# Optimization experiments

Measured on AMD Instinct MI355X. Metric: run time of the kernel, lower is better.

Reference implementation:

```python
import jax, jax.numpy as jnp
import numpy as np

N = 200000      # active voxels
G = 256         # dense grid extent per axis
C = 64          # inc = cs[0] at cr=1.0
S = 8           # aux pooling scale -> 32^3 aux cells
GS = G // S
NSEG = GS * GS * GS
EPS = 1e-6


def layernorm(x, w, b):
    m = jnp.mean(x, axis=-1, keepdims=True)
    v = jnp.mean((x - m) ** 2, axis=-1, keepdims=True)
    return (x - m) / jnp.sqrt(v + EPS) * w + b


def setup_inputs() -> dict:
    key = jax.random.key(0)
    ks = jax.random.split(key, 8)
    # unique voxel coordinates in a 256^3 grid (batch idx last, = 0)
    rng = np.random.default_rng(0)
    lin = rng.choice(G ** 3, size=N, replace=False).astype(np.int64)
    x = (lin // (G * G)).astype(np.int32)
    y = ((lin // G) % G).astype(np.int32)
    z = (lin % G).astype(np.int32)
    coords = jnp.asarray(np.stack([x, y, z, np.zeros(N, np.int32)], axis=1))
    feats = jax.random.normal(ks[0], (N, C), dtype=jnp.float32)
    return {
        "feats": feats,
        "W_pre": jax.random.normal(ks[1], (C, C), dtype=jnp.float32) * 0.05,
        "ln_pre_w": jnp.ones((C,), jnp.float32),
        "ln_pre_b": jnp.zeros((C,), jnp.float32),
        "W_pos": jax.random.normal(ks[2], (C, 3), dtype=jnp.float32) * 0.05,
        "alpha": jnp.ones((1, C), jnp.float32),
        "conv_w": jax.random.normal(ks[3], (27, C, C), dtype=jnp.float32) * 0.02,
        "ln_w": jnp.ones((C,), jnp.float32),
        "ln_b": jnp.zeros((C,), jnp.float32),
        "lnl_w": jnp.ones((C,), jnp.float32),
        "lnl_b": jnp.zeros((C,), jnp.float32),
        "coords": coords,
    }


def _elk_forward(feats, W_pre, ln_pre_w, ln_pre_b, W_pos, alpha, conv_w,
                 ln_w, ln_b, lnl_w, lnl_b, coords):
    xyz = coords[:, :3]
    # pre_mix: Linear(no bias) + LayerNorm
    F_input = layernorm(feats @ W_pre.T, ln_pre_w, ln_pre_b)
    # pos_weight = Linear(3->C, no bias)(xyz) * alpha (baseop='cos_x', groups=1)
    pos = (xyz.astype(jnp.float32) @ W_pos.T) * alpha          # [N, C]
    p_sin = jnp.sin(pos)
    p_cos = jnp.cos(pos)
    Fw_lin = F_input * pos
    # local_mix: 3x3x3 sparse conv on original feats via hash-grid gather
    gx, gy, gz = xyz[:, 0], xyz[:, 1], xyz[:, 2]
    grid = jnp.full((G, G, G), -1, jnp.int32).at[gx, gy, gz].set(
        jnp.arange(N, dtype=jnp.int32))
    local = jnp.zeros((N, C), jnp.float32)
    k = 0
    for dx in (-1, 0, 1):
        for dy in (-1, 0, 1):
            for dz in (-1, 0, 1):
                nc = xyz + jnp.array([dx, dy, dz], jnp.int32)
                inb = jnp.all((nc >= 0) & (nc < G), axis=1)
                ncc = jnp.clip(nc, 0, G - 1)
                nidx = grid[ncc[:, 0], ncc[:, 1], ncc[:, 2]]
                valid = inb & (nidx >= 0)
                g = jnp.where(valid[:, None],
                              feats[jnp.maximum(nidx, 0)], 0.0)
                local = local + g @ conv_w[k]
                k += 1
    # voxel_to_aux: scatter-pool the concat [cos*F, sin*F, pos*F] to aux cells
    stF = jnp.concatenate([F_input * p_cos, F_input * p_sin, Fw_lin], axis=1)
    cell = xyz // S
    seg = (cell[:, 0] * GS + cell[:, 1]) * GS + cell[:, 2]    # [N]
    sums = jax.ops.segment_sum(stF, seg, num_segments=NSEG)   # [NSEG, 3C]
    counts = jax.ops.segment_sum(jnp.ones((N,), jnp.float32), seg,
                                 num_segments=NSEG)
    # aux_to_voxel: broadcast aux mean back to each voxel
    vox = sums[seg] / jnp.maximum(counts[seg], 1.0)[:, None]  # [N, 3C]
    new_F = (vox[:, :C] * p_cos + vox[:, C:2 * C] * p_sin
             + (vox[:, 2 * C:] - Fw_lin))
    out = jax.nn.relu(layernorm(new_F, ln_w, ln_b)
                      + layernorm(local, lnl_w, lnl_b))
    return out


def reference(feats, W_pre, ln_pre_w, ln_pre_b, W_pos, alpha, conv_w,
              ln_w, ln_b, lnl_w, lnl_b, coords):
    return _elk_forward(feats, W_pre, ln_pre_w, ln_pre_b, W_pos, alpha,
                        conv_w, ln_w, ln_b, lnl_w, lnl_b, coords)
```

## Files before the change

### kernel.cpp

```cpp
#include <hip/hip_runtime.h>


typedef unsigned int u32;
typedef unsigned long long u64;

#define EPSV 1e-6f
#define HBITS 19
#define HSIZE (1u << HBITS)
#define HMASK (HSIZE - 1u)
#define CAP 32
#define PAD 65

template<int C,int R> __device__ __forceinline__ float dpp_add(float x){
    int y = __builtin_amdgcn_update_dpp(0, __float_as_int(x), C, R, 0xf, true);
    return x + __int_as_float(y);
}
__device__ __forceinline__ float wave_sum(float x){
    x = dpp_add<0xB1,0xF>(x);
    x = dpp_add<0x4E,0xF>(x);
    x = dpp_add<0x141,0xF>(x);
    x = dpp_add<0x140,0xF>(x);
    x = dpp_add<0x142,0xA>(x);
    x = dpp_add<0x143,0xC>(x);
    return __int_as_float(__builtin_amdgcn_readlane(__float_as_int(x), 63));
}
__device__ __forceinline__ void wave_sum2(float& x, float& y){
    x = dpp_add<0xB1,0xF>(x);   y = dpp_add<0xB1,0xF>(y);
    x = dpp_add<0x4E,0xF>(x);   y = dpp_add<0x4E,0xF>(y);
    x = dpp_add<0x141,0xF>(x);  y = dpp_add<0x141,0xF>(y);
    x = dpp_add<0x140,0xF>(x);  y = dpp_add<0x140,0xF>(y);
    x = dpp_add<0x142,0xA>(x);  y = dpp_add<0x142,0xA>(y);
    x = dpp_add<0x143,0xC>(x);  y = dpp_add<0x143,0xC>(y);
    x = __int_as_float(__builtin_amdgcn_readlane(__float_as_int(x), 63));
    y = __int_as_float(__builtin_amdgcn_readlane(__float_as_int(y), 63));
}

__device__ __forceinline__ u32 hslot(u32 b){ return (b * 0x9E3779B1u) >> (32 - HBITS); }

__global__ void k_scatter(const int* __restrict__ coords, u64* __restrict__ hash,
                          u32* __restrict__ bm, int n){
    int i = blockIdx.x * blockDim.x + threadIdx.x;
    if(i < n){
        int4 c = ((const int4*)coords)[i];
        u32 b = ((u32)c.x << 16) | ((u32)c.y << 8) | (u32)c.z;
        atomicOr(&bm[b >> 5], 1u << (b & 31));
        u64 entry = ((u64)b << 32) | (u32)i;
        u32 s = hslot(b);
        while(atomicCAS(&hash[s], ~0ull, entry) != ~0ull) s = (s + 1) & HMASK;
    }
}

__global__ void k_wtr(const float* __restrict__ W_pre, float* __restrict__ WT){
    for(int idx = threadIdx.x; idx < 4096; idx += 256){
        int j = idx >> 6, c = idx & 63;
        WT[j*64 + c] = W_pre[c*64 + j];
    }
}

__launch_bounds__(256, 2)
__global__ void k_preT(const float* __restrict__ feats, const float* __restrict__ WT,
                       const float* __restrict__ conv_w,
                       const float* __restrict__ lnw, const float* __restrict__ lnb,
                       float* __restrict__ F_input, float* __restrict__ selfconv, int n){
    __shared__ float T[64 * PAD];
    __shared__ float redm[4][64];
    __shared__ float redv[4][64];

    const int tid  = threadIdx.x;
    const int lane = tid & 63;
    const int wid  = tid >> 6;
    const int tbase = blockIdx.x << 6;

#pragma unroll
    for(int r = 0; r < 4; ++r){
        int idx = (r << 8) + tid;
        int pt = idx >> 4, j4 = idx & 15;
        float4 v = make_float4(0.f,0.f,0.f,0.f);
        if(tbase + pt < n) v = ((const float4*)feats)[(size_t)(tbase + pt) * 16 + j4];
        T[(4*j4 + 0)*PAD + pt] = v.x;
        T[(4*j4 + 1)*PAD + pt] = v.y;
        T[(4*j4 + 2)*PAD + pt] = v.z;
        T[(4*j4 + 3)*PAD + pt] = v.w;
    }
    __syncthreads();

    const int c0 = __builtin_amdgcn_readfirstlane(wid) << 4;
    const float* wa = WT + c0;
    const float* wb = conv_w + 13*4096 + c0;

    float accA[16], accB[16];
#pragma unroll
    for(int cc = 0; cc < 16; ++cc){ accA[cc] = 0.f; accB[cc] = 0.f; }

#pragma unroll 4
    for(int j = 0; j < 64; ++j){
        float v = T[j*PAD + lane];
        const float* waj = wa + j*64;
        const float* wbj = wb + j*64;
#pragma unroll
        for(int cc = 0; cc < 16; ++cc){
            accA[cc] = fmaf(v, waj[cc], accA[cc]);
            accB[cc] = fmaf(v, wbj[cc], accB[cc]);
        }
    }

    float s = 0.f;
#pragma unroll
    for(int cc = 0; cc < 16; ++cc) s += accA[cc];
    redm[wid][lane] = s;
    __syncthreads();
    const float mean = (redm[0][lane] + redm[1][lane] + redm[2][lane] + redm[3][lane]) * (1.f/64.f);
    float vs = 0.f;
#pragma unroll
    for(int cc = 0; cc < 16; ++cc){ float d = accA[cc] - mean; vs = fmaf(d, d, vs); }
    redv[wid][lane] = vs;
    __syncthreads();
    const float var = (redv[0][lane] + redv[1][lane] + redv[2][lane] + redv[3][lane]) * (1.f/64.f);
    const float rs = rsqrtf(var + EPSV);

#pragma unroll
    for(int cc = 0; cc < 16; ++cc)
        T[(c0 + cc)*PAD + lane] = (accA[cc] - mean) * rs * lnw[c0 + cc] + lnb[c0 + cc];
    __syncthreads();
#pragma unroll
    for(int r = 0; r < 4; ++r){
        int idx = (r << 8) + tid;
        int pt = idx >> 4, g = idx & 15;
        if(tbase + pt < n){
            float4 v = make_float4(T[(4*g+0)*PAD + pt], T[(4*g+1)*PAD + pt],
                                   T[(4*g+2)*PAD + pt], T[(4*g+3)*PAD + pt]);
            ((float4*)F_input)[(size_t)(tbase + pt) * 16 + g] = v;
        }
    }
    __syncthreads();

#pragma unroll
    for(int cc = 0; cc < 16; ++cc)
        T[(c0 + cc)*PAD + lane] = accB[cc];
    __syncthreads();
#pragma unroll
    for(int r = 0; r < 4; ++r){
        int idx = (r << 8) + tid;
        int pt = idx >> 4, g = idx & 15;
        if(tbase + pt < n){
            float4 v = make_float4(T[(4*g+0)*PAD + pt], T[(4*g+1)*PAD + pt],
                                   T[(4*g+2)*PAD + pt], T[(4*g+3)*PAD + pt]);
            ((float4*)selfconv)[(size_t)(tbase + pt) * 16 + g] = v;
        }
    }
}

__launch_bounds__(256)
__global__ void k_segfinal(const float* __restrict__ F_input,
                           const float* __restrict__ selfconv,
                           const float* __restrict__ feats,
                           const float* __restrict__ W_pos, const float* __restrict__ alpha,
                           const float* __restrict__ conv_w,
                           const float* __restrict__ ln_w, const float* __restrict__ ln_b,
                           const float* __restrict__ lnl_w, const float* __restrict__ lnl_b,
                           const u64* __restrict__ hash, const u32* __restrict__ bm,
                           float* __restrict__ out){
    __shared__ u32   s_pid[4][CAP];
    __shared__ u32   s_cell[4][CAP];
    __shared__ float s_v[4][3][64];
    __shared__ int   s_np[4];

    const u64* bm64 = (const u64*)bm;
    const int lane = threadIdx.x & 63;
    const int wid  = threadIdx.x >> 6;
    const int seg  = (blockIdx.x << 2) + wid;
    const int cx = seg >> 10, cy = (seg >> 5) & 31, cz = seg & 31;

    const int px = (cx << 3) + (lane >> 3), py = (cy << 3) + (lane & 7);
    u64 w = bm64[((size_t)px << 10) | ((u32)py << 2) | (u32)(cz >> 3)];
    u32 o8 = (u32)(w >> ((cz & 7) * 8)) & 0xffu;

    const float wx = W_pos[lane*3+0], wy = W_pos[lane*3+1], wz = W_pos[lane*3+2];
    const float al = alpha[lane];

    float aC = 0.f, aS = 0.f, aL = 0.f;
    int np = 0;
    float cnt = wave_sum((float)__popc(o8));
    u32 t8 = o8;
    while(__ballot(t8 != 0u)){
        int myz = 0, pid = -1;
        if(t8){
            int dz = __ffs(t8) - 1; t8 &= t8 - 1;
            myz = (cz << 3) + dz;
            u32 b = ((u32)px << 16) | ((u32)py << 8) | (u32)myz;
            u32 s = hslot(b); u64 e;
            while((u32)((e = hash[s]) >> 32) != b) s = (s + 1) & HMASK;
            pid = (int)(u32)e;
        }
        u64 mm = __ballot(pid >= 0);
        while(mm){
            int l = __ffsll(mm) - 1; mm &= mm - 1;
            int p  = __builtin_amdgcn_readlane(pid, l);
            int pz = __builtin_amdgcn_readlane(myz, l);
            int qx = (cx << 3) + (l >> 3), qy = (cy << 3) + (l & 7);
            if(np < CAP && lane == 0){
                s_pid[wid][np]  = (u32)p;
                s_cell[wid][np] = ((u32)qx << 16) | ((u32)qy << 8) | (u32)pz;
            }
            ++np;
            float F = F_input[(size_t)p * 64 + lane];
            float pos = ((float)qx*wx + (float)qy*wy + (float)pz*wz) * al;
            aC = fmaf(F, __cosf(pos), aC);
            aS = fmaf(F, __sinf(pos), aS);
            aL = fmaf(F, pos, aL);
        }
    }
    const float inv = 1.f / fmaxf(cnt, 1.f);
    s_v[wid][0][lane] = aC * inv;
    s_v[wid][1][lane] = aS * inv;
    s_v[wid][2][lane] = aL * inv;
    if(lane == 0) s_np[wid] = np < CAP ? np : CAP;
    __syncthreads();

    const float lnwv = ln_w[lane], lnbv = ln_b[lane];
    const float llwv = lnl_w[lane], llbv = lnl_b[lane];

    const int np0 = s_np[0], np1 = s_np[1], np2 = s_np[2], np3 = s_np[3];
    const int c01 = np0 + np1, c012 = c01 + np2;
    const int tot = c012 + np3;

    for(int idx = wid; idx < tot; idx += 4){
        int s, p;
        if(idx < np0){ s = 0; p = idx; }
        else if(idx < c01){ s = 1; p = idx - np0; }
        else if(idx < c012){ s = 2; p = idx - c01; }
        else { s = 3; p = idx - c012; }
        const u32 pid  = s_pid[s][p];
        const u32 cell = s_cell[s][p];
        const int qx = (int)(cell >> 16), qy = (int)((cell >> 8) & 255u), pz = (int)(cell & 255u);
        const float vCv = s_v[s][0][lane], vSv = s_v[s][1][lane], vLv = s_v[s][2][lane];

        float F  = F_input[(size_t)pid * 64 + lane];
        float Sc = selfconv[(size_t)pid * 64 + lane];

        u32 m3 = 0;
        if(lane < 9){
            int nx = qx + lane/3 - 1, ny = qy + lane%3 - 1;
            if(((u32)nx < 256u) && ((u32)ny < 256u)){
                const u64* wp = bm64 + (((size_t)nx << 10) | ((u32)ny << 2));
                int zb = pz & 63;
                if(zb >= 1 && zb <= 62){
                    u64 ww = wp[pz >> 6];
                    m3 = (u32)((ww >> (zb - 1)) & 7ull);
                } else {
#pragma unroll
                    for(int t = 0; t < 3; ++t){
                        int zz = pz + t - 1;
                        if((u32)zz < 256u){
                            u64 ww = wp[zz >> 6];
                            m3 |= (u32)((ww >> (zz & 63)) & 1ull) << t;
                        }
                    }
                }
            }
        }
        u64 b0m = __ballot(m3 & 1u);
        u64 b1m = __ballot(m3 & 2u) & ~(1ull << 4);
        u64 b2m = __ballot(m3 & 4u);

        float pos = ((float)qx*wx + (float)qy*wy + (float)pz*wz) * al;
        float sn = __sinf(pos), cs = __cosf(pos);
        float newF = fmaf(vCv, cs, fmaf(vSv, sn, vLv - F*pos));
        float local = Sc;

#pragma unroll
        for(int t = 0; t < 3; ++t){
            u64 mm2 = (t == 0) ? b0m : ((t == 1) ? b1m : b2m);
            while(mm2){
                int l2 = __ffsll(mm2) - 1; mm2 &= mm2 - 1;
                int nx = qx + l2/3 - 1, ny = qy + l2%3 - 1, nz = pz + t - 1;
                int k = 3*l2 + t;
                u32 nb = ((u32)nx << 16) | ((u32)ny << 8) | (u32)nz;
                u32 s2 = hslot(nb); u64 e;
                while((u32)((e = hash[s2]) >> 32) != nb) s2 = (s2 + 1) & HMASK;
                const int pin = (int)(u32)e;
                const float4* gv = (const float4*)(feats + (size_t)pin * 64);
                const float* cwp = conv_w + (size_t)k * 4096;
#pragma unroll 4
                for(int q = 0; q < 16; ++q){
                    float4 g = gv[q];
                    local = fmaf(g.x, cwp[(4*q    )*64 + lane], local);
                    local = fmaf(g.y, cwp[(4*q + 1)*64 + lane], local);
                    local = fmaf(g.z, cwp[(4*q + 2)*64 + lane], local);
                    local = fmaf(g.w, cwp[(4*q + 3)*64 + lane], local);
                }
            }
        }

        float m1 = newF, m2 = local;
        wave_sum2(m1, m2); m1 *= (1.f/64.f); m2 *= (1.f/64.f);
        float t1 = newF - m1, t2 = local - m2;
        float v1 = t1*t1, v2 = t2*t2;
        wave_sum2(v1, v2); v1 *= (1.f/64.f); v2 *= (1.f/64.f);
        float a1 = t1 * rsqrtf(v1 + EPSV) * lnwv + lnbv;
        float a2 = t2 * rsqrtf(v2 + EPSV) * llwv + llbv;

        out[(size_t)pid*64 + lane] = fmaxf(a1 + a2, 0.f);
    }
}

extern "C" void kernel_launch(void* const* d_in, const int* in_sizes, int n_in,
                              void* d_out, int out_size, void* d_ws, size_t ws_size,
                              hipStream_t stream) {
    (void)n_in; (void)out_size; (void)ws_size;
    const float* feats    = (const float*)d_in[0];
    const float* W_pre    = (const float*)d_in[1];
    const float* ln_pre_w = (const float*)d_in[2];
    const float* ln_pre_b = (const float*)d_in[3];
    const float* W_pos    = (const float*)d_in[4];
    const float* alpha    = (const float*)d_in[5];
    const float* conv_w   = (const float*)d_in[6];
    const float* ln_w     = (const float*)d_in[7];
    const float* ln_b     = (const float*)d_in[8];
    const float* lnl_w    = (const float*)d_in[9];
    const float* lnl_b    = (const float*)d_in[10];
    const int*   coords   = (const int*)d_in[11];

    const int n = in_sizes[0] / 64;

    char* ws = (char*)d_ws;
    size_t o = 0;
    u64*   hash    = (u64*)(ws + o);   o += (size_t)HSIZE * 8;
    u32*   bm      = (u32*)(ws + o);   o += 2097152;
    float* WT      = (float*)(ws + o); o += 16384;
    float* F_input = (float*)(ws + o); o += (size_t)n * 256;
    float* selfconv= (float*)(ws + o); o += (size_t)n * 256;

    hipMemsetAsync(hash, 0xFF, (size_t)HSIZE * 8, stream);
    hipMemsetAsync(bm, 0, 2097152, stream);

    k_wtr<<<1, 256, 0, stream>>>(W_pre, WT);
    k_scatter<<<(n + 255)/256, 256, 0, stream>>>(coords, hash, bm, n);
    k_preT<<<(n + 63)/64, 256, 0, stream>>>(feats, WT, conv_w, ln_pre_w, ln_pre_b,
                                            F_input, selfconv, n);
    k_segfinal<<<8192, 256, 0, stream>>>(F_input, selfconv, feats, W_pos, alpha,
                                         conv_w, ln_w, ln_b, lnl_w, lnl_b,
                                         hash, bm, (float*)d_out);
}
```

Measured before the change: 203.8 us.

## Fuse hash build into pre-mix kernel and cache gathered features in LDS

Result: slower. 221.9 us (+8.9%).

```diff
diff --git a/kernel.cpp b/kernel.cpp
--- a/kernel.cpp
+++ b/kernel.cpp
@@ -14,15 +14,6 @@
 template<int C,int R> __device__ __forceinline__ float dpp_add(float x){
     int y = __builtin_amdgcn_update_dpp(0, __float_as_int(x), C, R, 0xf, true);
     return x + __int_as_float(y);
-}
-__device__ __forceinline__ float wave_sum(float x){
-    x = dpp_add<0xB1,0xF>(x);
-    x = dpp_add<0x4E,0xF>(x);
-    x = dpp_add<0x141,0xF>(x);
-    x = dpp_add<0x140,0xF>(x);
-    x = dpp_add<0x142,0xA>(x);
-    x = dpp_add<0x143,0xC>(x);
-    return __int_as_float(__builtin_amdgcn_readlane(__float_as_int(x), 63));
 }
 __device__ __forceinline__ void wave_sum2(float& x, float& y){
     x = dpp_add<0xB1,0xF>(x);   y = dpp_add<0xB1,0xF>(y);
@@ -37,19 +28,6 @@
 
 __device__ __forceinline__ u32 hslot(u32 b){ return (b * 0x9E3779B1u) >> (32 - HBITS); }
 
-__global__ void k_scatter(const int* __restrict__ coords, u64* __restrict__ hash,
-                          u32* __restrict__ bm, int n){
-    int i = blockIdx.x * blockDim.x + threadIdx.x;
-    if(i < n){
-        int4 c = ((const int4*)coords)[i];
-        u32 b = ((u32)c.x << 16) | ((u32)c.y << 8) | (u32)c.z;
-        atomicOr(&bm[b >> 5], 1u << (b & 31));
-        u64 entry = ((u64)b << 32) | (u32)i;
-        u32 s = hslot(b);
-        while(atomicCAS(&hash[s], ~0ull, entry) != ~0ull) s = (s + 1) & HMASK;
-    }
-}
-
 __global__ void k_wtr(const float* __restrict__ W_pre, float* __restrict__ WT){
     for(int idx = threadIdx.x; idx < 4096; idx += 256){
         int j = idx >> 6, c = idx & 63;
@@ -61,6 +39,8 @@
 __global__ void k_preT(const float* __restrict__ feats, const float* __restrict__ WT,
                        const float* __restrict__ conv_w,
                        const float* __restrict__ lnw, const float* __restrict__ lnb,
+                       const int* __restrict__ coords,
+                       u64* __restrict__ hash, u32* __restrict__ bm,
                        float* __restrict__ F_input, float* __restrict__ selfconv, int n){
     __shared__ float T[64 * PAD];
     __shared__ float redm[4][64];
@@ -81,6 +61,15 @@
         T[(4*j4 + 1)*PAD + pt] = v.y;
         T[(4*j4 + 2)*PAD + pt] = v.z;
         T[(4*j4 + 3)*PAD + pt] = v.w;
+    }
+
+    if(tid < 64 && tbase + tid < n){
+        int4 c = ((const int4*)coords)[tbase + tid];
+        u32 b = ((u32)c.x << 16) | ((u32)c.y << 8) | (u32)c.z;
+        atomicOr(&bm[b >> 5], 1u << (b & 31));
+        u64 entry = ((u64)b << 32) | (u32)(tbase + tid);
+        u32 s = hslot(b);
+        while(atomicCAS(&hash[s], ~0ull, entry) != ~0ull) s = (s + 1) & HMASK;
     }
     __syncthreads();
 
@@ -160,6 +149,7 @@
                            const float* __restrict__ lnl_w, const float* __restrict__ lnl_b,
                            const u64* __restrict__ hash, const u32* __restrict__ bm,
                            float* __restrict__ out){
+    __shared__ float s_F[4][CAP][64];
     __shared__ u32   s_pid[4][CAP];
     __shared__ u32   s_cell[4][CAP];
     __shared__ float s_v[4][3][64];
@@ -178,49 +168,52 @@
     const float wx = W_pos[lane*3+0], wy = W_pos[lane*3+1], wz = W_pos[lane*3+2];
     const float al = alpha[lane];
 
+    if(lane == 0) s_np[wid] = 0;
+    __syncthreads();
+
+    u32 t8 = o8;
+    while(t8){
+        int dz = __ffs(t8) - 1; t8 &= t8 - 1;
+        int pz = (cz << 3) + dz;
+        u32 b = ((u32)px << 16) | ((u32)py << 8) | (u32)pz;
+        u32 s = hslot(b); u64 e;
+        while((u32)((e = hash[s]) >> 32) != b) s = (s + 1) & HMASK;
+        int slot = atomicAdd(&s_np[wid], 1);
+        if(slot < CAP){
+            s_pid[wid][slot]  = (u32)e;
+            s_cell[wid][slot] = b;
+        }
+    }
+    __syncthreads();
+
+    const int npAll = s_np[wid];
+    const int np = npAll < CAP ? npAll : CAP;
     float aC = 0.f, aS = 0.f, aL = 0.f;
-    int np = 0;
-    float cnt = wave_sum((float)__popc(o8));
-    u32 t8 = o8;
-    while(__ballot(t8 != 0u)){
-        int myz = 0, pid = -1;
-        if(t8){
-            int dz = __ffs(t8) - 1; t8 &= t8 - 1;
-            myz = (cz << 3) + dz;
-            u32 b = ((u32)px << 16) | ((u32)py << 8) | (u32)myz;
-            u32 s = hslot(b); u64 e;
-            while((u32)((e = hash[s]) >> 32) != b) s = (s + 1) & HMASK;
-            pid = (int)(u32)e;
-        }
-        u64 mm = __ballot(pid >= 0);
-        while(mm){
-            int l = __ffsll(mm) - 1; mm &= mm - 1;
-            int p  = __builtin_amdgcn_readlane(pid, l);
-            int pz = __builtin_amdgcn_readlane(myz, l);
-            int qx = (cx << 3) + (l >> 3), qy = (cy << 3) + (l & 7);
-            if(np < CAP && lane == 0){
-                s_pid[wid][np]  = (u32)p;
-                s_cell[wid][np] = ((u32)qx << 16) | ((u32)qy << 8) | (u32)pz;
-            }
-            ++np;
-            float F = F_input[(size_t)p * 64 + lane];
-            float pos = ((float)qx*wx + (float)qy*wy + (float)pz*wz) * al;
-            aC = fmaf(F, __cosf(pos), aC);
-            aS = fmaf(F, __sinf(pos), aS);
-            aL = fmaf(F, pos, aL);
-        }
-    }
-    const float inv = 1.f / fmaxf(cnt, 1.f);
+#pragma unroll 2
+    for(int p = 0; p < np; ++p){
+        const u32 pid  = s_pid[wid][p];
+        const u32 cell = s_cell[wid][p];
+        const int qx = (int)(cell >> 16), qy = (int)((cell >> 8) & 255u), pz = (int)(cell & 255u);
+        float F = F_input[(size_t)pid * 64 + lane];
+        s_F[wid][p][lane] = F;
+        float pos = ((float)qx*wx + (float)qy*wy + (float)pz*wz) * al;
+        aC = fmaf(F, __cosf(pos), aC);
+        aS = fmaf(F, __sinf(pos), aS);
+        aL = fmaf(F, pos, aL);
+    }
+    const float inv = 1.f / fmaxf((float)npAll, 1.f);
     s_v[wid][0][lane] = aC * inv;
     s_v[wid][1][lane] = aS * inv;
     s_v[wid][2][lane] = aL * inv;
-    if(lane == 0) s_np[wid] = np < CAP ? np : CAP;
     __syncthreads();
 
     const float lnwv = ln_w[lane], lnbv = ln_b[lane];
     const float llwv = lnl_w[lane], llbv = lnl_b[lane];
 
-    const int np0 = s_np[0], np1 = s_np[1], np2 = s_np[2], np3 = s_np[3];
+    const int np0 = s_np[0] < CAP ? s_np[0] : CAP;
+    const int np1 = s_np[1] < CAP ? s_np[1] : CAP;
+    const int np2 = s_np[2] < CAP ? s_np[2] : CAP;
+    const int np3 = s_np[3] < CAP ? s_np[3] : CAP;
     const int c01 = np0 + np1, c012 = c01 + np2;
     const int tot = c012 + np3;
 
@@ -235,7 +228,7 @@
         const int qx = (int)(cell >> 16), qy = (int)((cell >> 8) & 255u), pz = (int)(cell & 255u);
         const float vCv = s_v[s][0][lane], vSv = s_v[s][1][lane], vLv = s_v[s][2][lane];
 
-        float F  = F_input[(size_t)pid * 64 + lane];
+        float F  = s_F[s][p][lane];
         float Sc = selfconv[(size_t)pid * 64 + lane];
 
         u32 m3 = 0;
@@ -335,9 +328,8 @@
     hipMemsetAsync(bm, 0, 2097152, stream);
 
     k_wtr<<<1, 256, 0, stream>>>(W_pre, WT);
-    k_scatter<<<(n + 255)/256, 256, 0, stream>>>(coords, hash, bm, n);
     k_preT<<<(n + 63)/64, 256, 0, stream>>>(feats, WT, conv_w, ln_pre_w, ln_pre_b,
-                                            F_input, selfconv, n);
+                                            coords, hash, bm, F_input, selfconv, n);
     k_segfinal<<<8192, 256, 0, stream>>>(F_input, selfconv, feats, W_pos, alpha,
                                          conv_w, ln_w, ln_b, lnl_w, lnl_b,
                                          hash, bm, (float*)d_out);
```
